# Performance work log

Measured on AMD Instinct MI355X. Metric: run time of the kernel, lower is better.

## Reference

```python
import jax, jax.numpy as jnp
import numpy as np

B, H, HF = 2048, 128, 10  # batch, bi-LSTM hidden, fc-LSTM hidden


def _lstm(x_seq, h0, c0, Wih, Whh, bih, bhh):
    """Unidirectional LSTM, PyTorch gate order (i, f, g, o).
    x_seq: [T, B, I]. Returns final (h, c), each [B, H].
    Input projection is hoisted out of the scan (one big GEMM)."""
    pre = jnp.einsum('tbi,gi->tbg', x_seq, Wih) + bih + bhh  # [T, B, 4H]

    def step(carry, p):
        h, c = carry
        g = p + h @ Whh.T
        i, f, gg, o = jnp.split(g, 4, axis=-1)
        c = jax.nn.sigmoid(f) * c + jax.nn.sigmoid(i) * jnp.tanh(gg)
        h = jax.nn.sigmoid(o) * jnp.tanh(c)
        return (h, c), None

    (hT, cT), _ = jax.lax.scan(step, (h0, c0), pre)
    return hT, cT


def setup_inputs() -> dict:
    key = jax.random.key(0)
    ks = iter(jax.random.split(key, 40))
    s = 1.0 / np.sqrt(H)
    sf = 1.0 / np.sqrt(HF)
    u = lambda shape, sc: jax.random.uniform(next(ks), shape, jnp.float32, -sc, sc)
    inp = {"x": jax.random.normal(next(ks), (B, 28, 28), jnp.float32)}
    for name in ["lr_f", "lr_b", "ud_f", "ud_b"]:
        inp["Wih_" + name] = u((4 * H, 28), s)
        inp["Whh_" + name] = u((4 * H, H), s)
        inp["bih_" + name] = u((4 * H,), s)
        inp["bhh_" + name] = u((4 * H,), s)
    inp["Wih_fc"] = u((4 * HF, 1), sf)
    inp["Whh_fc"] = u((4 * HF, HF), sf)
    inp["bih_fc"] = u((4 * HF,), sf)
    inp["bhh_fc"] = u((4 * HF,), sf)
    for name in ["h0_lr", "c0_lr", "h0_ud", "c0_ud"]:
        inp[name] = jax.random.normal(next(ks), (2, B, H), jnp.float32)
    inp["h0_fc"] = jax.random.normal(next(ks), (B, HF), jnp.float32)
    inp["c0_fc"] = jax.random.normal(next(ks), (B, HF), jnp.float32)
    return inp


def reference(x, Wih_lr_f, Whh_lr_f, bih_lr_f, bhh_lr_f,
              Wih_lr_b, Whh_lr_b, bih_lr_b, bhh_lr_b,
              Wih_ud_f, Whh_ud_f, bih_ud_f, bhh_ud_f,
              Wih_ud_b, Whh_ud_b, bih_ud_b, bhh_ud_b,
              Wih_fc, Whh_fc, bih_fc, bhh_fc,
              h0_lr, c0_lr, h0_ud, c0_ud, h0_fc, c0_fc):
    x_lr = jnp.transpose(x, (1, 0, 2))  # [28, B, 28]: rows as time
    x_ud = jnp.transpose(x, (2, 0, 1))  # [28, B, 28]: cols as time
    # bidirectional = forward scan + scan over reversed sequence
    h_lr_f, _ = _lstm(x_lr, h0_lr[0], c0_lr[0], Wih_lr_f, Whh_lr_f, bih_lr_f, bhh_lr_f)
    h_lr_b, _ = _lstm(x_lr[::-1], h0_lr[1], c0_lr[1], Wih_lr_b, Whh_lr_b, bih_lr_b, bhh_lr_b)
    h_ud_f, _ = _lstm(x_ud, h0_ud[0], c0_ud[0], Wih_ud_f, Whh_ud_f, bih_ud_f, bhh_ud_f)
    h_ud_b, _ = _lstm(x_ud[::-1], h0_ud[1], c0_ud[1], Wih_ud_b, Whh_ud_b, bih_ud_b, bhh_ud_b)
    feat = jnp.concatenate([h_lr_f, h_lr_b, h_ud_f, h_ud_b], axis=1)  # [B, 4H]
    seq = feat.T[:, :, None]  # [4H, B, 1]: feature index is the fc-LSTM time axis
    h_f, _ = _lstm(seq, h0_fc, c0_fc, Wih_fc, Whh_fc, bih_fc, bhh_fc)  # [B, 10]
    return jax.nn.log_softmax(h_f, axis=1)
```

## Files before the change

### kernel.cpp

```cpp
#include <hip/hip_runtime.h>
#include <hip/hip_bf16.h>

typedef __bf16 bf16x8 __attribute__((ext_vector_type(8)));
typedef float  f32x4  __attribute__((ext_vector_type(4)));

#define LOG2E 1.4426950408889634f
#define LN2   0.6931471805599453f

__device__ __forceinline__ float rcp_(float x){
#if __has_builtin(__builtin_amdgcn_rcpf)
  return __builtin_amdgcn_rcpf(x);
#else
  return 1.0f / x;
#endif
}
__device__ __forceinline__ float ex2_(float x){
#if __has_builtin(__builtin_amdgcn_exp2f)
  return __builtin_amdgcn_exp2f(x);
#else
  return exp2f(x);
#endif
}
__device__ __forceinline__ float lg2_(float x){
#if __has_builtin(__builtin_amdgcn_logf)
  return __builtin_amdgcn_logf(x);
#else
  return log2f(x);
#endif
}
__device__ __forceinline__ float sigp_(float xp){ return rcp_(1.0f + ex2_(xp)); }
__device__ __forceinline__ float tanp_(float gp){ return 1.0f - 2.0f*rcp_(1.0f + ex2_(gp)); }

struct LstmArgs {
  const float* Wih[4]; const float* Whh[4];
  const float* bih[4]; const float* bhh[4];
  const float* h0[4];  const float* c0[4];
};

__global__ void pack_weights(LstmArgs args, bf16x8* __restrict__ wpack,
                             float* __restrict__ bpack)
{
  const int idx = blockIdx.x*256 + threadIdx.x;
  if (idx >= 4*8*4*5*64) return;
  const int lane = idx & 63;
  int r = idx >> 6;
  const int kk = r % 5; r /= 5;
  const int g  = r & 3; r >>= 2;
  const int w  = r & 7;
  const int d  = r >> 3;
  const int lc = lane & 15, lr4 = lane >> 4;
  const int grow = g*128 + w*16 + lc;
  const float sc = (g == 2) ? 2.0f*LOG2E : -LOG2E;

  bf16x8 v;
  if (kk < 4){
    const float* p = args.Whh[d] + grow*128 + kk*32 + lr4*8;
#pragma unroll
    for (int j = 0; j < 8; ++j) v[j] = (__bf16)(p[j] * sc);
  } else {
#pragma unroll
    for (int j = 0; j < 8; ++j){
      const int xi = lr4*8 + j;
      v[j] = (xi < 28) ? (__bf16)(args.Wih[d][grow*28 + xi] * sc) : (__bf16)0.0f;
    }
  }
  wpack[idx] = v;
  if (kk == 0 && lr4 == 0)
    bpack[d*512 + grow] = (args.bih[d][grow] + args.bhh[d][grow]) * sc;
}

__global__ __launch_bounds__(512, 2) void lstm4_kernel(const float* __restrict__ x,
                                                       LstmArgs args,
                                                       const bf16x8* __restrict__ wpack,
                                                       const float* __restrict__ bpack,
                                                       __bf16* __restrict__ featB)
{
  const int dir = blockIdx.x >> 6;
  const int b0  = (blockIdx.x & 63) * 32;
  const int tid = threadIdx.x;
  const int w   = tid >> 6;
  const int l   = tid & 63;
  const int lc  = l & 15;
  const int lr4 = l >> 4;

  const float* __restrict__ h0 = args.h0[dir];
  const float* __restrict__ c0 = args.c0[dir];
  const int rev = dir & 1;
  const bool lrdir = (dir < 2);

  __shared__ __align__(16) __bf16 hcat[32 * 168];
  __shared__ __align__(16) __bf16 xstage[28 * 32 * 40];

  bf16x8 bfr[4][5];
  float  bias[4];
  {
    const bf16x8* wp = wpack + (dir*8 + w)*4*5*64;
#pragma unroll
    for (int g = 0; g < 4; ++g){
#pragma unroll
      for (int kk = 0; kk < 5; ++kk)
        bfr[g][kk] = wp[(g*5 + kk)*64 + l];
      bias[g] = bpack[dir*512 + g*128 + w*16 + lc];
    }
  }

  for (int idx = tid; idx < 32*196; idx += 512){
    const int row = idx / 196;
    const int rem = idx - row*196;
    if (lrdir){
      const int t = rem / 7, jg = rem - 7*t;
      const float4 v = *(const float4*)&x[(b0+row)*784 + t*28 + jg*4];
      __bf16* dst = &xstage[(t*32 + row)*40 + jg*4];
      dst[0]=(__bf16)v.x; dst[1]=(__bf16)v.y; dst[2]=(__bf16)v.z; dst[3]=(__bf16)v.w;
    } else {
      const int j = rem / 7, tg = rem - 7*j;
      const float4 v = *(const float4*)&x[(b0+row)*784 + j*28 + tg*4];
      xstage[((tg*4+0)*32 + row)*40 + j] = (__bf16)v.x;
      xstage[((tg*4+1)*32 + row)*40 + j] = (__bf16)v.y;
      xstage[((tg*4+2)*32 + row)*40 + j] = (__bf16)v.z;
      xstage[((tg*4+3)*32 + row)*40 + j] = (__bf16)v.w;
    }
  }
  for (int idx = tid; idx < 28*32; idx += 512){
    const int t = idx >> 5, row = idx & 31;
    __bf16* p = &xstage[(t*32 + row)*40 + 28];
    p[0] = p[1] = p[2] = p[3] = (__bf16)0.0f;
  }

  float cst[2][4], hfin[2][4];
#pragma unroll
  for (int m = 0; m < 2; ++m)
#pragma unroll
  for (int r = 0; r < 4; ++r){
    const int row = 16*m + 4*lr4 + r;
    const int col = w*16 + lc;
    cst[m][r] = c0[(b0+row)*128 + col];
    hcat[row*168 + col] = (__bf16)h0[(b0+row)*128 + col];
    hfin[m][r] = 0.0f;
  }

  for (int s = 0; s < 28; ++s){
    const int t = rev ? (27 - s) : s;
    __syncthreads();

    f32x4 acc[2][4];
#pragma unroll
    for (int m = 0; m < 2; ++m)
#pragma unroll
    for (int g = 0; g < 4; ++g){
      f32x4 bv = {bias[g], bias[g], bias[g], bias[g]};
      acc[m][g] = bv;
    }
#pragma unroll
    for (int m = 0; m < 2; ++m){
#pragma unroll
      for (int kk = 0; kk < 5; ++kk){
        const bf16x8 a = (kk < 4)
          ? *(const bf16x8*)&hcat[(16*m + lc)*168 + kk*32 + lr4*8]
          : *(const bf16x8*)&xstage[(t*32 + 16*m + lc)*40 + lr4*8];
#pragma unroll
        for (int g = 0; g < 4; ++g)
          acc[m][g] = __builtin_amdgcn_mfma_f32_16x16x32_bf16(a, bfr[g][kk], acc[m][g], 0, 0, 0);
      }
    }
    __syncthreads();

#pragma unroll
    for (int m = 0; m < 2; ++m)
#pragma unroll
    for (int r = 0; r < 4; ++r){
      const float cc = sigp_(acc[m][1][r])*cst[m][r] + sigp_(acc[m][0][r])*tanp_(acc[m][2][r]);
      cst[m][r] = cc;
      const float hv = sigp_(acc[m][3][r])*tanp_(2.0f*LOG2E*cc);
      hfin[m][r] = hv;
      hcat[(16*m + 4*lr4 + r)*168 + w*16 + lc] = (__bf16)hv;
    }
  }

  {
    const int fcol = dir*128 + w*16 + lc;
#pragma unroll
    for (int m = 0; m < 2; ++m)
#pragma unroll
    for (int r = 0; r < 4; ++r)
      featB[(b0 + 16*m + 4*lr4 + r)*512 + fcol] = (__bf16)hfin[m][r];
  }
}

__global__ __launch_bounds__(256) void fc_lstm_wave(const ushort* __restrict__ featB,
                                                    const float* __restrict__ Wih,
                                                    const float* __restrict__ Whh,
                                                    const float* __restrict__ bih,
                                                    const float* __restrict__ bhh,
                                                    const float* __restrict__ h0,
                                                    const float* __restrict__ c0,
                                                    float* __restrict__ out)
{
  const int tid = threadIdx.x;
  const int l   = tid & 63;
  const int e   = blockIdx.x*4 + (tid >> 6);
  const int u   = l >> 2;
  const int g   = l & 3;
  const int uc  = (u < 10) ? u : 9;
  const bool valid = (u < 10);
  const float sc = (g == 2) ? 2.0f*LOG2E : -LOG2E;
  const int row = g*10 + uc;

  float wh[10];
#pragma unroll
  for (int m = 0; m < 10; ++m) wh[m] = valid ? Whh[row*10 + m]*sc : 0.0f;
  const float wx   = valid ? Wih[row]*sc : 0.0f;
  const float bia  = valid ? (bih[row] + bhh[row])*sc : 0.0f;
  const float actA = (g == 2) ? 1.0f : 0.0f;
  const float actB = (g == 2) ? -2.0f : 1.0f;

  float c = valid ? c0[e*10 + uc] : 0.0f;
  float hlast = valid ? h0[e*10 + uc] : 0.0f;

  int hb = __float_as_int(hlast);
  float sh0 = __int_as_float(__builtin_amdgcn_readlane(hb,  0));
  float sh1 = __int_as_float(__builtin_amdgcn_readlane(hb,  4));
  float sh2 = __int_as_float(__builtin_amdgcn_readlane(hb,  8));
  float sh3 = __int_as_float(__builtin_amdgcn_readlane(hb, 12));
  float sh4 = __int_as_float(__builtin_amdgcn_readlane(hb, 16));
  float sh5 = __int_as_float(__builtin_amdgcn_readlane(hb, 20));
  float sh6 = __int_as_float(__builtin_amdgcn_readlane(hb, 24));
  float sh7 = __int_as_float(__builtin_amdgcn_readlane(hb, 28));
  float sh8 = __int_as_float(__builtin_amdgcn_readlane(hb, 32));
  float sh9 = __int_as_float(__builtin_amdgcn_readlane(hb, 36));

  const ushort* fB = featB + e*512;
  int vxc = (int)fB[l];
  int vxn = (int)fB[64 + l];

  for (int win = 0; win < 8; ++win){
#pragma unroll 4
    for (int j = 0; j < 64; ++j){
      const float xs = __int_as_float(__builtin_amdgcn_readlane(vxc, j) << 16);
      float a0 = __builtin_fmaf(wx, xs, bia);
      a0 = __builtin_fmaf(wh[0], sh0, a0);
      float a1 = wh[1]*sh1;
      a0 = __builtin_fmaf(wh[2], sh2, a0); a1 = __builtin_fmaf(wh[3], sh3, a1);
      a0 = __builtin_fmaf(wh[4], sh4, a0); a1 = __builtin_fmaf(wh[5], sh5, a1);
      a0 = __builtin_fmaf(wh[6], sh6, a0); a1 = __builtin_fmaf(wh[7], sh7, a1);
      a0 = __builtin_fmaf(wh[8], sh8, a0); a1 = __builtin_fmaf(wh[9], sh9, a1);
      const float acc = a0 + a1;
      const float rc  = rcp_(1.0f + ex2_(acc));
      const float val = __builtin_fmaf(actB, rc, actA);
      const int   vi  = __float_as_int(val);
      const float si  = __int_as_float(__builtin_amdgcn_mov_dpp(vi, 0x00, 0xF, 0xF, false));
      const float sf  = __int_as_float(__builtin_amdgcn_mov_dpp(vi, 0x55, 0xF, 0xF, false));
      const float tg  = __int_as_float(__builtin_amdgcn_mov_dpp(vi, 0xAA, 0xF, 0xF, false));
      const float so  = __int_as_float(__builtin_amdgcn_mov_dpp(vi, 0xFF, 0xF, 0xF, false));
      c = __builtin_fmaf(sf, c, si*tg);
      const float tc = __builtin_fmaf(-2.0f, rcp_(1.0f + ex2_(2.0f*LOG2E*c)), 1.0f);
      const float h  = so*tc;
      hlast = h;
      const int hbi = __float_as_int(h);
      sh0 = __int_as_float(__builtin_amdgcn_readlane(hbi,  0));
      sh1 = __int_as_float(__builtin_amdgcn_readlane(hbi,  4));
      sh2 = __int_as_float(__builtin_amdgcn_readlane(hbi,  8));
      sh3 = __int_as_float(__builtin_amdgcn_readlane(hbi, 12));
      sh4 = __int_as_float(__builtin_amdgcn_readlane(hbi, 16));
      sh5 = __int_as_float(__builtin_amdgcn_readlane(hbi, 20));
      sh6 = __int_as_float(__builtin_amdgcn_readlane(hbi, 24));
      sh7 = __int_as_float(__builtin_amdgcn_readlane(hbi, 28));
      sh8 = __int_as_float(__builtin_amdgcn_readlane(hbi, 32));
      sh9 = __int_as_float(__builtin_amdgcn_readlane(hbi, 36));
    }
    vxc = vxn;
    if (win < 6) vxn = (int)fB[(win+2)*64 + l];
  }

  float mx = sh0;
  mx = fmaxf(mx, sh1); mx = fmaxf(mx, sh2); mx = fmaxf(mx, sh3);
  mx = fmaxf(mx, sh4); mx = fmaxf(mx, sh5); mx = fmaxf(mx, sh6);
  mx = fmaxf(mx, sh7); mx = fmaxf(mx, sh8); mx = fmaxf(mx, sh9);
  float es = ex2_(LOG2E*(sh0 - mx));
  es += ex2_(LOG2E*(sh1 - mx)); es += ex2_(LOG2E*(sh2 - mx));
  es += ex2_(LOG2E*(sh3 - mx)); es += ex2_(LOG2E*(sh4 - mx));
  es += ex2_(LOG2E*(sh5 - mx)); es += ex2_(LOG2E*(sh6 - mx));
  es += ex2_(LOG2E*(sh7 - mx)); es += ex2_(LOG2E*(sh8 - mx));
  es += ex2_(LOG2E*(sh9 - mx));
  const float lse = LN2 * lg2_(es);
  if (valid && g == 0) out[e*10 + u] = hlast - mx - lse;
}

extern "C" void kernel_launch(void* const* d_in, const int* in_sizes, int n_in,
                              void* d_out, int out_size, void* d_ws, size_t ws_size,
                              hipStream_t stream)
{
  const float* x = (const float*)d_in[0];
  LstmArgs a;
  const int base[4] = {1, 5, 9, 13};
  for (int d = 0; d < 4; ++d){
    a.Wih[d] = (const float*)d_in[base[d] + 0];
    a.Whh[d] = (const float*)d_in[base[d] + 1];
    a.bih[d] = (const float*)d_in[base[d] + 2];
    a.bhh[d] = (const float*)d_in[base[d] + 3];
  }
  const float* h0lr = (const float*)d_in[21];
  const float* c0lr = (const float*)d_in[22];
  const float* h0ud = (const float*)d_in[23];
  const float* c0ud = (const float*)d_in[24];
  a.h0[0] = h0lr;               a.c0[0] = c0lr;
  a.h0[1] = h0lr + 2048*128;    a.c0[1] = c0lr + 2048*128;
  a.h0[2] = h0ud;               a.c0[2] = c0ud;
  a.h0[3] = h0ud + 2048*128;    a.c0[3] = c0ud + 2048*128;

  char* ws = (char*)d_ws;
  __bf16* featB = (__bf16*)ws;
  bf16x8* wpack = (bf16x8*)(ws + (2u<<20));
  float*  bpack = (float*)(ws + (2u<<20) + 655360u);

  pack_weights<<<160, 256, 0, stream>>>(a, wpack, bpack);
  lstm4_kernel<<<256, 512, 0, stream>>>(x, a, wpack, bpack, featB);
  fc_lstm_wave<<<512, 256, 0, stream>>>((const ushort*)featB,
      (const float*)d_in[17], (const float*)d_in[18],
      (const float*)d_in[19], (const float*)d_in[20],
      (const float*)d_in[25], (const float*)d_in[26],
      (float*)d_out);
}
```

Measured before the change: 142.1 us.

## Halve LSTM batch tile with double-buffered h, interleave two fc-LSTM sequences per wave

The bi-LSTM kernel now handles 16 batch rows per block instead of 32, launching twice as many blocks at higher occupancy. The hidden-state buffer is double-buffered so each timestep needs one barrier instead of two. The fc-LSTM kernel now runs two independent sequences per wave, interleaved to hide the latency of the serial recurrence, and launches half as many blocks. The cost is more per-wave register pressure in the fc kernel and per-block fixed overhead (weight fragment loads) paid twice as often in the bi-LSTM kernel.

Measured after the change: 160.4 us. 12.9% more time.

```diff
diff --git a/kernel.cpp b/kernel.cpp
--- a/kernel.cpp
+++ b/kernel.cpp
@@ -69,14 +69,14 @@
     bpack[d*512 + grow] = (args.bih[d][grow] + args.bhh[d][grow]) * sc;
 }
 
-__global__ __launch_bounds__(512, 2) void lstm4_kernel(const float* __restrict__ x,
+__global__ __launch_bounds__(512, 4) void lstm4_kernel(const float* __restrict__ x,
                                                        LstmArgs args,
                                                        const bf16x8* __restrict__ wpack,
                                                        const float* __restrict__ bpack,
                                                        __bf16* __restrict__ featB)
 {
-  const int dir = blockIdx.x >> 6;
-  const int b0  = (blockIdx.x & 63) * 32;
+  const int dir = blockIdx.x >> 7;
+  const int b0  = (blockIdx.x & 127) * 16;
   const int tid = threadIdx.x;
   const int w   = tid >> 6;
   const int l   = tid & 63;
@@ -88,8 +88,8 @@
   const int rev = dir & 1;
   const bool lrdir = (dir < 2);
 
-  __shared__ __align__(16) __bf16 hcat[32 * 168];
-  __shared__ __align__(16) __bf16 xstage[28 * 32 * 40];
+  __shared__ __align__(16) __bf16 hcat[2][16 * 168];
+  __shared__ __align__(16) __bf16 xstage[28 * 16 * 40];
 
   bf16x8 bfr[4][5];
   float  bias[4];
@@ -104,86 +104,77 @@
     }
   }
 
-  for (int idx = tid; idx < 32*196; idx += 512){
+  for (int idx = tid; idx < 16*196; idx += 512){
     const int row = idx / 196;
     const int rem = idx - row*196;
     if (lrdir){
       const int t = rem / 7, jg = rem - 7*t;
       const float4 v = *(const float4*)&x[(b0+row)*784 + t*28 + jg*4];
-      __bf16* dst = &xstage[(t*32 + row)*40 + jg*4];
+      __bf16* dst = &xstage[(t*16 + row)*40 + jg*4];
       dst[0]=(__bf16)v.x; dst[1]=(__bf16)v.y; dst[2]=(__bf16)v.z; dst[3]=(__bf16)v.w;
     } else {
       const int j = rem / 7, tg = rem - 7*j;
       const float4 v = *(const float4*)&x[(b0+row)*784 + j*28 + tg*4];
-      xstage[((tg*4+0)*32 + row)*40 + j] = (__bf16)v.x;
-      xstage[((tg*4+1)*32 + row)*40 + j] = (__bf16)v.y;
-      xstage[((tg*4+2)*32 + row)*40 + j] = (__bf16)v.z;
-      xstage[((tg*4+3)*32 + row)*40 + j] = (__bf16)v.w;
-    }
-  }
-  for (int idx = tid; idx < 28*32; idx += 512){
-    const int t = idx >> 5, row = idx & 31;
-    __bf16* p = &xstage[(t*32 + row)*40 + 28];
+      xstage[((tg*4+0)*16 + row)*40 + j] = (__bf16)v.x;
+      xstage[((tg*4+1)*16 + row)*40 + j] = (__bf16)v.y;
+      xstage[((tg*4+2)*16 + row)*40 + j] = (__bf16)v.z;
+      xstage[((tg*4+3)*16 + row)*40 + j] = (__bf16)v.w;
+    }
+  }
+  if (tid < 28*16){
+    const int t = tid >> 4, row = tid & 15;
+    __bf16* p = &xstage[(t*16 + row)*40 + 28];
     p[0] = p[1] = p[2] = p[3] = (__bf16)0.0f;
   }
 
-  float cst[2][4], hfin[2][4];
-#pragma unroll
-  for (int m = 0; m < 2; ++m)
+  float cst[4], hfin[4];
 #pragma unroll
   for (int r = 0; r < 4; ++r){
-    const int row = 16*m + 4*lr4 + r;
+    const int row = 4*lr4 + r;
     const int col = w*16 + lc;
-    cst[m][r] = c0[(b0+row)*128 + col];
-    hcat[row*168 + col] = (__bf16)h0[(b0+row)*128 + col];
-    hfin[m][r] = 0.0f;
-  }
-
+    cst[r] = c0[(b0+row)*128 + col];
+    hcat[0][row*168 + col] = (__bf16)h0[(b0+row)*128 + col];
+    hfin[r] = 0.0f;
+  }
+  __syncthreads();
+
+  int cur = 0;
   for (int s = 0; s < 28; ++s){
     const int t = rev ? (27 - s) : s;
-    __syncthreads();
-
-    f32x4 acc[2][4];
-#pragma unroll
-    for (int m = 0; m < 2; ++m)
+
+    f32x4 acc[4];
 #pragma unroll
     for (int g = 0; g < 4; ++g){
       f32x4 bv = {bias[g], bias[g], bias[g], bias[g]};
-      acc[m][g] = bv;
-    }
-#pragma unroll
-    for (int m = 0; m < 2; ++m){
-#pragma unroll
-      for (int kk = 0; kk < 5; ++kk){
-        const bf16x8 a = (kk < 4)
-          ? *(const bf16x8*)&hcat[(16*m + lc)*168 + kk*32 + lr4*8]
-          : *(const bf16x8*)&xstage[(t*32 + 16*m + lc)*40 + lr4*8];
-#pragma unroll
-        for (int g = 0; g < 4; ++g)
-          acc[m][g] = __builtin_amdgcn_mfma_f32_16x16x32_bf16(a, bfr[g][kk], acc[m][g], 0, 0, 0);
-      }
+      acc[g] = bv;
+    }
+#pragma unroll
+    for (int kk = 0; kk < 5; ++kk){
+      const bf16x8 a = (kk < 4)
+        ? *(const bf16x8*)&hcat[cur][lc*168 + kk*32 + lr4*8]
+        : *(const bf16x8*)&xstage[(t*16 + lc)*40 + lr4*8];
+#pragma unroll
+      for (int g = 0; g < 4; ++g)
+        acc[g] = __builtin_amdgcn_mfma_f32_16x16x32_bf16(a, bfr[g][kk], acc[g], 0, 0, 0);
+    }
+
+#pragma unroll
+    for (int r = 0; r < 4; ++r){
+      const float cc = sigp_(acc[1][r])*cst[r] + sigp_(acc[0][r])*tanp_(acc[2][r]);
+      cst[r] = cc;
+      const float hv = sigp_(acc[3][r])*tanp_(2.0f*LOG2E*cc);
+      hfin[r] = hv;
+      hcat[cur^1][(4*lr4 + r)*168 + w*16 + lc] = (__bf16)hv;
     }
     __syncthreads();
-
-#pragma unroll
-    for (int m = 0; m < 2; ++m)
-#pragma unroll
-    for (int r = 0; r < 4; ++r){
-      const float cc = sigp_(acc[m][1][r])*cst[m][r] + sigp_(acc[m][0][r])*tanp_(acc[m][2][r]);
-      cst[m][r] = cc;
-      const float hv = sigp_(acc[m][3][r])*tanp_(2.0f*LOG2E*cc);
-      hfin[m][r] = hv;
-      hcat[(16*m + 4*lr4 + r)*168 + w*16 + lc] = (__bf16)hv;
-    }
+    cur ^= 1;
   }
 
   {
     const int fcol = dir*128 + w*16 + lc;
 #pragma unroll
-    for (int m = 0; m < 2; ++m)
-#pragma unroll
     for (int r = 0; r < 4; ++r)
-      featB[(b0 + 16*m + 4*lr4 + r)*512 + fcol] = (__bf16)hfin[m][r];
+      featB[(b0 + 4*lr4 + r)*512 + fcol] = (__bf16)hfin[r];
   }
 }
 
@@ -198,7 +189,7 @@
 {
   const int tid = threadIdx.x;
   const int l   = tid & 63;
-  const int e   = blockIdx.x*4 + (tid >> 6);
+  const int e0  = (blockIdx.x*4 + (tid >> 6)) * 2;
   const int u   = l >> 2;
   const int g   = l & 3;
   const int uc  = (u < 10) ? u : 9;
@@ -214,76 +205,71 @@
   const float actA = (g == 2) ? 1.0f : 0.0f;
   const float actB = (g == 2) ? -2.0f : 1.0f;
 
-  float c = valid ? c0[e*10 + uc] : 0.0f;
-  float hlast = valid ? h0[e*10 + uc] : 0.0f;
-
-  int hb = __float_as_int(hlast);
-  float sh0 = __int_as_float(__builtin_amdgcn_readlane(hb,  0));
-  float sh1 = __int_as_float(__builtin_amdgcn_readlane(hb,  4));
-  float sh2 = __int_as_float(__builtin_amdgcn_readlane(hb,  8));
-  float sh3 = __int_as_float(__builtin_amdgcn_readlane(hb, 12));
-  float sh4 = __int_as_float(__builtin_amdgcn_readlane(hb, 16));
-  float sh5 = __int_as_float(__builtin_amdgcn_readlane(hb, 20));
-  float sh6 = __int_as_float(__builtin_amdgcn_readlane(hb, 24));
-  float sh7 = __int_as_float(__builtin_amdgcn_readlane(hb, 28));
-  float sh8 = __int_as_float(__builtin_amdgcn_readlane(hb, 32));
-  float sh9 = __int_as_float(__builtin_amdgcn_readlane(hb, 36));
-
-  const ushort* fB = featB + e*512;
-  int vxc = (int)fB[l];
-  int vxn = (int)fB[64 + l];
+  float c[2], hlast[2];
+  float sh[2][10];
+  int   vxc[2], vxn[2];
+#pragma unroll
+  for (int E = 0; E < 2; ++E){
+    const int e = e0 + E;
+    c[E]     = valid ? c0[e*10 + uc] : 0.0f;
+    hlast[E] = valid ? h0[e*10 + uc] : 0.0f;
+    const int hb = __float_as_int(hlast[E]);
+#pragma unroll
+    for (int m = 0; m < 10; ++m)
+      sh[E][m] = __int_as_float(__builtin_amdgcn_readlane(hb, 4*m));
+    vxc[E] = (int)featB[e*512 + l];
+    vxn[E] = (int)featB[e*512 + 64 + l];
+  }
 
   for (int win = 0; win < 8; ++win){
-#pragma unroll 4
+#pragma unroll 2
     for (int j = 0; j < 64; ++j){
-      const float xs = __int_as_float(__builtin_amdgcn_readlane(vxc, j) << 16);
-      float a0 = __builtin_fmaf(wx, xs, bia);
-      a0 = __builtin_fmaf(wh[0], sh0, a0);
-      float a1 = wh[1]*sh1;
-      a0 = __builtin_fmaf(wh[2], sh2, a0); a1 = __builtin_fmaf(wh[3], sh3, a1);
-      a0 = __builtin_fmaf(wh[4], sh4, a0); a1 = __builtin_fmaf(wh[5], sh5, a1);
-      a0 = __builtin_fmaf(wh[6], sh6, a0); a1 = __builtin_fmaf(wh[7], sh7, a1);
-      a0 = __builtin_fmaf(wh[8], sh8, a0); a1 = __builtin_fmaf(wh[9], sh9, a1);
-      const float acc = a0 + a1;
-      const float rc  = rcp_(1.0f + ex2_(acc));
-      const float val = __builtin_fmaf(actB, rc, actA);
-      const int   vi  = __float_as_int(val);
-      const float si  = __int_as_float(__builtin_amdgcn_mov_dpp(vi, 0x00, 0xF, 0xF, false));
-      const float sf  = __int_as_float(__builtin_amdgcn_mov_dpp(vi, 0x55, 0xF, 0xF, false));
-      const float tg  = __int_as_float(__builtin_amdgcn_mov_dpp(vi, 0xAA, 0xF, 0xF, false));
-      const float so  = __int_as_float(__builtin_amdgcn_mov_dpp(vi, 0xFF, 0xF, 0xF, false));
-      c = __builtin_fmaf(sf, c, si*tg);
-      const float tc = __builtin_fmaf(-2.0f, rcp_(1.0f + ex2_(2.0f*LOG2E*c)), 1.0f);
-      const float h  = so*tc;
-      hlast = h;
-      const int hbi = __float_as_int(h);
-      sh0 = __int_as_float(__builtin_amdgcn_readlane(hbi,  0));
-      sh1 = __int_as_float(__builtin_amdgcn_readlane(hbi,  4));
-      sh2 = __int_as_float(__builtin_amdgcn_readlane(hbi,  8));
-      sh3 = __int_as_float(__builtin_amdgcn_readlane(hbi, 12));
-      sh4 = __int_as_float(__builtin_amdgcn_readlane(hbi, 16));
-      sh5 = __int_as_float(__builtin_amdgcn_readlane(hbi, 20));
-      sh6 = __int_as_float(__builtin_amdgcn_readlane(hbi, 24));
-      sh7 = __int_as_float(__builtin_amdgcn_readlane(hbi, 28));
-      sh8 = __int_as_float(__builtin_amdgcn_readlane(hbi, 32));
-      sh9 = __int_as_float(__builtin_amdgcn_readlane(hbi, 36));
-    }
-    vxc = vxn;
-    if (win < 6) vxn = (int)fB[(win+2)*64 + l];
-  }
-
-  float mx = sh0;
-  mx = fmaxf(mx, sh1); mx = fmaxf(mx, sh2); mx = fmaxf(mx, sh3);
-  mx = fmaxf(mx, sh4); mx = fmaxf(mx, sh5); mx = fmaxf(mx, sh6);
-  mx = fmaxf(mx, sh7); mx = fmaxf(mx, sh8); mx = fmaxf(mx, sh9);
-  float es = ex2_(LOG2E*(sh0 - mx));
-  es += ex2_(LOG2E*(sh1 - mx)); es += ex2_(LOG2E*(sh2 - mx));
-  es += ex2_(LOG2E*(sh3 - mx)); es += ex2_(LOG2E*(sh4 - mx));
-  es += ex2_(LOG2E*(sh5 - mx)); es += ex2_(LOG2E*(sh6 - mx));
-  es += ex2_(LOG2E*(sh7 - mx)); es += ex2_(LOG2E*(sh8 - mx));
-  es += ex2_(LOG2E*(sh9 - mx));
-  const float lse = LN2 * lg2_(es);
-  if (valid && g == 0) out[e*10 + u] = hlast - mx - lse;
+#pragma unroll
+      for (int E = 0; E < 2; ++E){
+        const float xs = __int_as_float(__builtin_amdgcn_readlane(vxc[E], j) << 16);
+        float a0 = __builtin_fmaf(wx, xs, bia);
+        a0 = __builtin_fmaf(wh[0], sh[E][0], a0);
+        float a1 = wh[1]*sh[E][1];
+        a0 = __builtin_fmaf(wh[2], sh[E][2], a0); a1 = __builtin_fmaf(wh[3], sh[E][3], a1);
+        a0 = __builtin_fmaf(wh[4], sh[E][4], a0); a1 = __builtin_fmaf(wh[5], sh[E][5], a1);
+        a0 = __builtin_fmaf(wh[6], sh[E][6], a0); a1 = __builtin_fmaf(wh[7], sh[E][7], a1);
+        a0 = __builtin_fmaf(wh[8], sh[E][8], a0); a1 = __builtin_fmaf(wh[9], sh[E][9], a1);
+        const float acc = a0 + a1;
+        const float rc  = rcp_(1.0f + ex2_(acc));
+        const float val = __builtin_fmaf(actB, rc, actA);
+        const int   vi  = __float_as_int(val);
+        const float si  = __int_as_float(__builtin_amdgcn_mov_dpp(vi, 0x00, 0xF, 0xF, false));
+        const float sf  = __int_as_float(__builtin_amdgcn_mov_dpp(vi, 0x55, 0xF, 0xF, false));
+        const float tg  = __int_as_float(__builtin_amdgcn_mov_dpp(vi, 0xAA, 0xF, 0xF, false));
+        const float so  = __int_as_float(__builtin_amdgcn_mov_dpp(vi, 0xFF, 0xF, 0xF, false));
+        c[E] = __builtin_fmaf(sf, c[E], si*tg);
+        const float tc = __builtin_fmaf(-2.0f, rcp_(1.0f + ex2_(2.0f*LOG2E*c[E])), 1.0f);
+        const float h  = so*tc;
+        hlast[E] = h;
+        const int hbi = __float_as_int(h);
+#pragma unroll
+        for (int m = 0; m < 10; ++m)
+          sh[E][m] = __int_as_float(__builtin_amdgcn_readlane(hbi, 4*m));
+      }
+    }
+#pragma unroll
+    for (int E = 0; E < 2; ++E){
+      vxc[E] = vxn[E];
+      if (win < 6) vxn[E] = (int)featB[(e0+E)*512 + (win+2)*64 + l];
+    }
+  }
+
+#pragma unroll
+  for (int E = 0; E < 2; ++E){
+    float mx = sh[E][0];
+#pragma unroll
+    for (int m = 1; m < 10; ++m) mx = fmaxf(mx, sh[E][m]);
+    float es = 0.0f;
+#pragma unroll
+    for (int m = 0; m < 10; ++m) es += ex2_(LOG2E*(sh[E][m] - mx));
+    const float lse = LN2 * lg2_(es);
+    if (valid && g == 0) out[(e0+E)*10 + u] = hlast[E] - mx - lse;
+  }
 }
 
 extern "C" void kernel_launch(void* const* d_in, const int* in_sizes, int n_in,
@@ -314,8 +300,8 @@
   float*  bpack = (float*)(ws + (2u<<20) + 655360u);
 
   pack_weights<<<160, 256, 0, stream>>>(a, wpack, bpack);
-  lstm4_kernel<<<256, 512, 0, stream>>>(x, a, wpack, bpack, featB);
-  fc_lstm_wave<<<512, 256, 0, stream>>>((const ushort*)featB,
+  lstm4_kernel<<<512, 512, 0, stream>>>(x, a, wpack, bpack, featB);
+  fc_lstm_wave<<<256, 256, 0, stream>>>((const ushort*)featB,
       (const float*)d_in[17], (const float*)d_in[18],
       (const float*)d_in[19], (const float*)d_in[20],
       (const float*)d_in[25], (const float*)d_in[26],
```

## Double-buffer hidden state, merge gate reciprocals, use packed fp16 dot in fc LSTM

Applied to the files above, without the earlier changes.

In the bi-LSTM kernel the hidden-state tile in shared memory is now double-buffered, which drops one of the two barriers per timestep. The gate math is reworked to share reciprocals across sigmoid/tanh pairs, and the final features are written with vectorized 16-byte stores taken from shared memory. In the fc LSTM the recurrent weights and hidden values are packed into fp16 pairs and combined with fdot2, halving the readlanes and FMAs on the serial critical path. The cost is reduced precision from fp16 round-toward-zero packing and a possible overflow risk when the exponentials are multiplied together.

Measured after the change: 139.7 us. About the same (-1.7%).

```diff
diff --git a/kernel.cpp b/kernel.cpp
--- a/kernel.cpp
+++ b/kernel.cpp
@@ -1,8 +1,9 @@
 #include <hip/hip_runtime.h>
 #include <hip/hip_bf16.h>
 
-typedef __bf16 bf16x8 __attribute__((ext_vector_type(8)));
-typedef float  f32x4  __attribute__((ext_vector_type(4)));
+typedef __bf16   bf16x8 __attribute__((ext_vector_type(8)));
+typedef float    f32x4  __attribute__((ext_vector_type(4)));
+typedef _Float16 h16x2  __attribute__((ext_vector_type(2)));
 
 #define LOG2E 1.4426950408889634f
 #define LN2   0.6931471805599453f
@@ -30,6 +31,25 @@
 }
 __device__ __forceinline__ float sigp_(float xp){ return rcp_(1.0f + ex2_(xp)); }
 __device__ __forceinline__ float tanp_(float gp){ return 1.0f - 2.0f*rcp_(1.0f + ex2_(gp)); }
+
+__device__ __forceinline__ int pkrtz_(float a, float b){
+  auto v = __builtin_amdgcn_cvt_pkrtz(a, b);
+  int r; __builtin_memcpy(&r, &v, 4); return r;
+}
+__device__ __forceinline__ h16x2 as_h2_(int x){
+  h16x2 r; __builtin_memcpy(&r, &x, 4); return r;
+}
+
+#if __has_builtin(__builtin_amdgcn_fdot2)
+__device__ __forceinline__ float fdot2_(int w, int h, float a){
+  return __builtin_amdgcn_fdot2(as_h2_(w), as_h2_(h), a, false);
+}
+#else
+__device__ __forceinline__ float fdot2_(int w, int h, float a){
+  h16x2 wv = as_h2_(w), hv = as_h2_(h);
+  return a + (float)wv[0]*(float)hv[0] + (float)wv[1]*(float)hv[1];
+}
+#endif
 
 struct LstmArgs {
   const float* Wih[4]; const float* Whh[4];
@@ -88,7 +108,7 @@
   const int rev = dir & 1;
   const bool lrdir = (dir < 2);
 
-  __shared__ __align__(16) __bf16 hcat[32 * 168];
+  __shared__ __align__(16) __bf16 hcat[2][32 * 168];
   __shared__ __align__(16) __bf16 xstage[28 * 32 * 40];
 
   bf16x8 bfr[4][5];
@@ -127,7 +147,7 @@
     p[0] = p[1] = p[2] = p[3] = (__bf16)0.0f;
   }
 
-  float cst[2][4], hfin[2][4];
+  float cst[2][4];
 #pragma unroll
   for (int m = 0; m < 2; ++m)
 #pragma unroll
@@ -135,13 +155,14 @@
     const int row = 16*m + 4*lr4 + r;
     const int col = w*16 + lc;
     cst[m][r] = c0[(b0+row)*128 + col];
-    hcat[row*168 + col] = (__bf16)h0[(b0+row)*128 + col];
-    hfin[m][r] = 0.0f;
-  }
-
+    hcat[0][row*168 + col] = (__bf16)h0[(b0+row)*128 + col];
+  }
+  __syncthreads();
+
+  int cur = 0;
   for (int s = 0; s < 28; ++s){
     const int t = rev ? (27 - s) : s;
-    __syncthreads();
+    const int nxt = cur ^ 1;
 
     f32x4 acc[2][4];
 #pragma unroll
@@ -156,34 +177,40 @@
 #pragma unroll
       for (int kk = 0; kk < 5; ++kk){
         const bf16x8 a = (kk < 4)
-          ? *(const bf16x8*)&hcat[(16*m + lc)*168 + kk*32 + lr4*8]
+          ? *(const bf16x8*)&hcat[cur][(16*m + lc)*168 + kk*32 + lr4*8]
           : *(const bf16x8*)&xstage[(t*32 + 16*m + lc)*40 + lr4*8];
 #pragma unroll
         for (int g = 0; g < 4; ++g)
           acc[m][g] = __builtin_amdgcn_mfma_f32_16x16x32_bf16(a, bfr[g][kk], acc[m][g], 0, 0, 0);
       }
     }
+
+#pragma unroll
+    for (int m = 0; m < 2; ++m)
+#pragma unroll
+    for (int r = 0; r < 4; ++r){
+      const float Ei = ex2_(acc[m][0][r]);
+      const float Ef = ex2_(acc[m][1][r]);
+      const float Eg = ex2_(acc[m][2][r]);
+      const float Eo = ex2_(acc[m][3][r]);
+      const float rf  = rcp_(1.0f + Ef);
+      const float rig = rcp_((1.0f + Ei)*(1.0f + Eg));
+      const float cc  = rf*cst[m][r] + (Eg - 1.0f)*rig;
+      cst[m][r] = cc;
+      const float Ec  = ex2_(2.0f*LOG2E*cc);
+      const float roc = rcp_((1.0f + Eo)*(1.0f + Ec));
+      const float hv  = (Ec - 1.0f)*roc;
+      hcat[nxt][(16*m + 4*lr4 + r)*168 + w*16 + lc] = (__bf16)hv;
+    }
     __syncthreads();
-
-#pragma unroll
-    for (int m = 0; m < 2; ++m)
-#pragma unroll
-    for (int r = 0; r < 4; ++r){
-      const float cc = sigp_(acc[m][1][r])*cst[m][r] + sigp_(acc[m][0][r])*tanp_(acc[m][2][r]);
-      cst[m][r] = cc;
-      const float hv = sigp_(acc[m][3][r])*tanp_(2.0f*LOG2E*cc);
-      hfin[m][r] = hv;
-      hcat[(16*m + 4*lr4 + r)*168 + w*16 + lc] = (__bf16)hv;
-    }
+    cur = nxt;
   }
 
   {
-    const int fcol = dir*128 + w*16 + lc;
-#pragma unroll
-    for (int m = 0; m < 2; ++m)
-#pragma unroll
-    for (int r = 0; r < 4; ++r)
-      featB[(b0 + 16*m + 4*lr4 + r)*512 + fcol] = (__bf16)hfin[m][r];
+    const int row = tid >> 4;
+    const int cg  = tid & 15;
+    const bf16x8 hv = *(const bf16x8*)&hcat[cur][row*168 + cg*8];
+    *(bf16x8*)&featB[(b0+row)*512 + dir*128 + cg*8] = hv;
   }
 }
 
@@ -206,28 +233,32 @@
   const float sc = (g == 2) ? 2.0f*LOG2E : -LOG2E;
   const int row = g*10 + uc;
 
-  float wh[10];
-#pragma unroll
-  for (int m = 0; m < 10; ++m) wh[m] = valid ? Whh[row*10 + m]*sc : 0.0f;
+  int wh2[5];
+#pragma unroll
+  for (int m = 0; m < 5; ++m){
+    const float w0 = valid ? Whh[row*10 + 2*m]   * sc : 0.0f;
+    const float w1 = valid ? Whh[row*10 + 2*m+1] * sc : 0.0f;
+    wh2[m] = pkrtz_(w0, w1);
+  }
   const float wx   = valid ? Wih[row]*sc : 0.0f;
   const float bia  = valid ? (bih[row] + bhh[row])*sc : 0.0f;
   const float actA = (g == 2) ? 1.0f : 0.0f;
   const float actB = (g == 2) ? -2.0f : 1.0f;
 
-  float c = valid ? c0[e*10 + uc] : 0.0f;
+  float c     = valid ? c0[e*10 + uc] : 0.0f;
   float hlast = valid ? h0[e*10 + uc] : 0.0f;
 
-  int hb = __float_as_int(hlast);
-  float sh0 = __int_as_float(__builtin_amdgcn_readlane(hb,  0));
-  float sh1 = __int_as_float(__builtin_amdgcn_readlane(hb,  4));
-  float sh2 = __int_as_float(__builtin_amdgcn_readlane(hb,  8));
-  float sh3 = __int_as_float(__builtin_amdgcn_readlane(hb, 12));
-  float sh4 = __int_as_float(__builtin_amdgcn_readlane(hb, 16));
-  float sh5 = __int_as_float(__builtin_amdgcn_readlane(hb, 20));
-  float sh6 = __int_as_float(__builtin_amdgcn_readlane(hb, 24));
-  float sh7 = __int_as_float(__builtin_amdgcn_readlane(hb, 28));
-  float sh8 = __int_as_float(__builtin_amdgcn_readlane(hb, 32));
-  float sh9 = __int_as_float(__builtin_amdgcn_readlane(hb, 36));
+  int hp0, hp1, hp2, hp3, hp4;
+  {
+    const float hnb = __int_as_float(
+        __builtin_amdgcn_ds_swizzle(__float_as_int(hlast), 0x101F));
+    const int hpi = pkrtz_(hlast, hnb);
+    hp0 = __builtin_amdgcn_readlane(hpi,  0);
+    hp1 = __builtin_amdgcn_readlane(hpi,  8);
+    hp2 = __builtin_amdgcn_readlane(hpi, 16);
+    hp3 = __builtin_amdgcn_readlane(hpi, 24);
+    hp4 = __builtin_amdgcn_readlane(hpi, 32);
+  }
 
   const ushort* fB = featB + e*512;
   int vxc = (int)fB[l];
@@ -238,12 +269,11 @@
     for (int j = 0; j < 64; ++j){
       const float xs = __int_as_float(__builtin_amdgcn_readlane(vxc, j) << 16);
       float a0 = __builtin_fmaf(wx, xs, bia);
-      a0 = __builtin_fmaf(wh[0], sh0, a0);
-      float a1 = wh[1]*sh1;
-      a0 = __builtin_fmaf(wh[2], sh2, a0); a1 = __builtin_fmaf(wh[3], sh3, a1);
-      a0 = __builtin_fmaf(wh[4], sh4, a0); a1 = __builtin_fmaf(wh[5], sh5, a1);
-      a0 = __builtin_fmaf(wh[6], sh6, a0); a1 = __builtin_fmaf(wh[7], sh7, a1);
-      a0 = __builtin_fmaf(wh[8], sh8, a0); a1 = __builtin_fmaf(wh[9], sh9, a1);
+      a0 = fdot2_(wh2[0], hp0, a0);
+      float a1 = fdot2_(wh2[1], hp1, 0.0f);
+      a0 = fdot2_(wh2[2], hp2, a0);
+      a1 = fdot2_(wh2[3], hp3, a1);
+      a0 = fdot2_(wh2[4], hp4, a0);
       const float acc = a0 + a1;
       const float rc  = rcp_(1.0f + ex2_(acc));
       const float val = __builtin_fmaf(actB, rc, actA);
@@ -256,32 +286,30 @@
       const float tc = __builtin_fmaf(-2.0f, rcp_(1.0f + ex2_(2.0f*LOG2E*c)), 1.0f);
       const float h  = so*tc;
       hlast = h;
-      const int hbi = __float_as_int(h);
-      sh0 = __int_as_float(__builtin_amdgcn_readlane(hbi,  0));
-      sh1 = __int_as_float(__builtin_amdgcn_readlane(hbi,  4));
-      sh2 = __int_as_float(__builtin_amdgcn_readlane(hbi,  8));
-      sh3 = __int_as_float(__builtin_amdgcn_readlane(hbi, 12));
-      sh4 = __int_as_float(__builtin_amdgcn_readlane(hbi, 16));
-      sh5 = __int_as_float(__builtin_amdgcn_readlane(hbi, 20));
-      sh6 = __int_as_float(__builtin_amdgcn_readlane(hbi, 24));
-      sh7 = __int_as_float(__builtin_amdgcn_readlane(hbi, 28));
-      sh8 = __int_as_float(__builtin_amdgcn_readlane(hbi, 32));
-      sh9 = __int_as_float(__builtin_amdgcn_readlane(hbi, 36));
+      const float hnb = __int_as_float(
+          __builtin_amdgcn_ds_swizzle(__float_as_int(h), 0x101F));
+      const int hpi = pkrtz_(h, hnb);
+      hp0 = __builtin_amdgcn_readlane(hpi,  0);
+      hp1 = __builtin_amdgcn_readlane(hpi,  8);
+      hp2 = __builtin_amdgcn_readlane(hpi, 16);
+      hp3 = __builtin_amdgcn_readlane(hpi, 24);
+      hp4 = __builtin_amdgcn_readlane(hpi, 32);
     }
     vxc = vxn;
     if (win < 6) vxn = (int)fB[(win+2)*64 + l];
   }
 
-  float mx = sh0;
-  mx = fmaxf(mx, sh1); mx = fmaxf(mx, sh2); mx = fmaxf(mx, sh3);
-  mx = fmaxf(mx, sh4); mx = fmaxf(mx, sh5); mx = fmaxf(mx, sh6);
-  mx = fmaxf(mx, sh7); mx = fmaxf(mx, sh8); mx = fmaxf(mx, sh9);
-  float es = ex2_(LOG2E*(sh0 - mx));
-  es += ex2_(LOG2E*(sh1 - mx)); es += ex2_(LOG2E*(sh2 - mx));
-  es += ex2_(LOG2E*(sh3 - mx)); es += ex2_(LOG2E*(sh4 - mx));
-  es += ex2_(LOG2E*(sh5 - mx)); es += ex2_(LOG2E*(sh6 - mx));
-  es += ex2_(LOG2E*(sh7 - mx)); es += ex2_(LOG2E*(sh8 - mx));
-  es += ex2_(LOG2E*(sh9 - mx));
+  const int hb = __float_as_int(hlast);
+  float sh[10];
+#pragma unroll
+  for (int m = 0; m < 10; ++m)
+    sh[m] = __int_as_float(__builtin_amdgcn_readlane(hb, 4*m));
+  float mx = sh[0];
+#pragma unroll
+  for (int m = 1; m < 10; ++m) mx = fmaxf(mx, sh[m]);
+  float es = 0.0f;
+#pragma unroll
+  for (int m = 0; m < 10; ++m) es += ex2_(LOG2E*(sh[m] - mx));
   const float lse = LN2 * lg2_(es);
   if (valid && g == 0) out[e*10 + u] = hlast - mx - lse;
 }
```

## Double-buffer LSTM hidden state, merge gate reciprocals, shorten fc dependency chain

Applied to the files above, without the earlier changes.

The bi-LSTM kernel now ping-pongs the hidden-state tile between two shared buffers, which removes one of the two per-step barriers. The gate math merges reciprocals by computing sigmoid(i)*tanh(g) and sigmoid(o)*tanh(c) with a single rcp on a product of denominators, cutting transcendental ops per element. Final features are written from shared memory with vectorized 16-byte stores instead of scattered scalar stores. In the fc LSTM, the 10-term dot product is split into four shorter FMA chains and the unroll factor is raised to 8; the merged reciprocals risk overflow when the exponentials become large.

New measurement: 137.7 us. -3.0%, faster.

```diff
diff --git a/kernel.cpp b/kernel.cpp
--- a/kernel.cpp
+++ b/kernel.cpp
@@ -1,8 +1,8 @@
 #include <hip/hip_runtime.h>
 #include <hip/hip_bf16.h>
 
-typedef __bf16 bf16x8 __attribute__((ext_vector_type(8)));
-typedef float  f32x4  __attribute__((ext_vector_type(4)));
+typedef __bf16   bf16x8 __attribute__((ext_vector_type(8)));
+typedef float    f32x4  __attribute__((ext_vector_type(4)));
 
 #define LOG2E 1.4426950408889634f
 #define LN2   0.6931471805599453f
@@ -28,8 +28,6 @@
   return log2f(x);
 #endif
 }
-__device__ __forceinline__ float sigp_(float xp){ return rcp_(1.0f + ex2_(xp)); }
-__device__ __forceinline__ float tanp_(float gp){ return 1.0f - 2.0f*rcp_(1.0f + ex2_(gp)); }
 
 struct LstmArgs {
   const float* Wih[4]; const float* Whh[4];
@@ -88,7 +86,7 @@
   const int rev = dir & 1;
   const bool lrdir = (dir < 2);
 
-  __shared__ __align__(16) __bf16 hcat[32 * 168];
+  __shared__ __align__(16) __bf16 hcat[2][32 * 168];
   __shared__ __align__(16) __bf16 xstage[28 * 32 * 40];
 
   bf16x8 bfr[4][5];
@@ -127,7 +125,7 @@
     p[0] = p[1] = p[2] = p[3] = (__bf16)0.0f;
   }
 
-  float cst[2][4], hfin[2][4];
+  float cst[2][4];
 #pragma unroll
   for (int m = 0; m < 2; ++m)
 #pragma unroll
@@ -135,13 +133,14 @@
     const int row = 16*m + 4*lr4 + r;
     const int col = w*16 + lc;
     cst[m][r] = c0[(b0+row)*128 + col];
-    hcat[row*168 + col] = (__bf16)h0[(b0+row)*128 + col];
-    hfin[m][r] = 0.0f;
-  }
-
+    hcat[0][row*168 + col] = (__bf16)h0[(b0+row)*128 + col];
+  }
+  __syncthreads();
+
+  int cur = 0;
   for (int s = 0; s < 28; ++s){
     const int t = rev ? (27 - s) : s;
-    __syncthreads();
+    const int nxt = cur ^ 1;
 
     f32x4 acc[2][4];
 #pragma unroll
@@ -156,34 +155,40 @@
 #pragma unroll
       for (int kk = 0; kk < 5; ++kk){
         const bf16x8 a = (kk < 4)
-          ? *(const bf16x8*)&hcat[(16*m + lc)*168 + kk*32 + lr4*8]
+          ? *(const bf16x8*)&hcat[cur][(16*m + lc)*168 + kk*32 + lr4*8]
           : *(const bf16x8*)&xstage[(t*32 + 16*m + lc)*40 + lr4*8];
 #pragma unroll
         for (int g = 0; g < 4; ++g)
           acc[m][g] = __builtin_amdgcn_mfma_f32_16x16x32_bf16(a, bfr[g][kk], acc[m][g], 0, 0, 0);
       }
     }
+
+#pragma unroll
+    for (int m = 0; m < 2; ++m)
+#pragma unroll
+    for (int r = 0; r < 4; ++r){
+      const float Ei = ex2_(acc[m][0][r]);
+      const float Ef = ex2_(acc[m][1][r]);
+      const float Eg = ex2_(acc[m][2][r]);
+      const float Eo = ex2_(acc[m][3][r]);
+      const float rf  = rcp_(1.0f + Ef);
+      const float rig = rcp_((1.0f + Ei)*(1.0f + Eg));
+      const float cc  = rf*cst[m][r] + (Eg - 1.0f)*rig;
+      cst[m][r] = cc;
+      const float Ec  = ex2_(2.0f*LOG2E*cc);
+      const float roc = rcp_((1.0f + Eo)*(1.0f + Ec));
+      const float hv  = (Ec - 1.0f)*roc;
+      hcat[nxt][(16*m + 4*lr4 + r)*168 + w*16 + lc] = (__bf16)hv;
+    }
     __syncthreads();
-
-#pragma unroll
-    for (int m = 0; m < 2; ++m)
-#pragma unroll
-    for (int r = 0; r < 4; ++r){
-      const float cc = sigp_(acc[m][1][r])*cst[m][r] + sigp_(acc[m][0][r])*tanp_(acc[m][2][r]);
-      cst[m][r] = cc;
-      const float hv = sigp_(acc[m][3][r])*tanp_(2.0f*LOG2E*cc);
-      hfin[m][r] = hv;
-      hcat[(16*m + 4*lr4 + r)*168 + w*16 + lc] = (__bf16)hv;
-    }
+    cur = nxt;
   }
 
   {
-    const int fcol = dir*128 + w*16 + lc;
-#pragma unroll
-    for (int m = 0; m < 2; ++m)
-#pragma unroll
-    for (int r = 0; r < 4; ++r)
-      featB[(b0 + 16*m + 4*lr4 + r)*512 + fcol] = (__bf16)hfin[m][r];
+    const int row = tid >> 4;
+    const int cg  = tid & 15;
+    const bf16x8 hv = *(const bf16x8*)&hcat[cur][row*168 + cg*8];
+    *(bf16x8*)&featB[(b0+row)*512 + dir*128 + cg*8] = hv;
   }
 }
 
@@ -214,37 +219,44 @@
   const float actA = (g == 2) ? 1.0f : 0.0f;
   const float actB = (g == 2) ? -2.0f : 1.0f;
 
-  float c = valid ? c0[e*10 + uc] : 0.0f;
+  float c     = valid ? c0[e*10 + uc] : 0.0f;
   float hlast = valid ? h0[e*10 + uc] : 0.0f;
 
-  int hb = __float_as_int(hlast);
-  float sh0 = __int_as_float(__builtin_amdgcn_readlane(hb,  0));
-  float sh1 = __int_as_float(__builtin_amdgcn_readlane(hb,  4));
-  float sh2 = __int_as_float(__builtin_amdgcn_readlane(hb,  8));
-  float sh3 = __int_as_float(__builtin_amdgcn_readlane(hb, 12));
-  float sh4 = __int_as_float(__builtin_amdgcn_readlane(hb, 16));
-  float sh5 = __int_as_float(__builtin_amdgcn_readlane(hb, 20));
-  float sh6 = __int_as_float(__builtin_amdgcn_readlane(hb, 24));
-  float sh7 = __int_as_float(__builtin_amdgcn_readlane(hb, 28));
-  float sh8 = __int_as_float(__builtin_amdgcn_readlane(hb, 32));
-  float sh9 = __int_as_float(__builtin_amdgcn_readlane(hb, 36));
+  float sh0, sh1, sh2, sh3, sh4, sh5, sh6, sh7, sh8, sh9;
+  {
+    const int hb = __float_as_int(hlast);
+    sh0 = __int_as_float(__builtin_amdgcn_readlane(hb,  0));
+    sh1 = __int_as_float(__builtin_amdgcn_readlane(hb,  4));
+    sh2 = __int_as_float(__builtin_amdgcn_readlane(hb,  8));
+    sh3 = __int_as_float(__builtin_amdgcn_readlane(hb, 12));
+    sh4 = __int_as_float(__builtin_amdgcn_readlane(hb, 16));
+    sh5 = __int_as_float(__builtin_amdgcn_readlane(hb, 20));
+    sh6 = __int_as_float(__builtin_amdgcn_readlane(hb, 24));
+    sh7 = __int_as_float(__builtin_amdgcn_readlane(hb, 28));
+    sh8 = __int_as_float(__builtin_amdgcn_readlane(hb, 32));
+    sh9 = __int_as_float(__builtin_amdgcn_readlane(hb, 36));
+  }
 
   const ushort* fB = featB + e*512;
   int vxc = (int)fB[l];
   int vxn = (int)fB[64 + l];
 
   for (int win = 0; win < 8; ++win){
-#pragma unroll 4
+#pragma unroll 8
     for (int j = 0; j < 64; ++j){
       const float xs = __int_as_float(__builtin_amdgcn_readlane(vxc, j) << 16);
       float a0 = __builtin_fmaf(wx, xs, bia);
       a0 = __builtin_fmaf(wh[0], sh0, a0);
-      float a1 = wh[1]*sh1;
-      a0 = __builtin_fmaf(wh[2], sh2, a0); a1 = __builtin_fmaf(wh[3], sh3, a1);
-      a0 = __builtin_fmaf(wh[4], sh4, a0); a1 = __builtin_fmaf(wh[5], sh5, a1);
-      a0 = __builtin_fmaf(wh[6], sh6, a0); a1 = __builtin_fmaf(wh[7], sh7, a1);
-      a0 = __builtin_fmaf(wh[8], sh8, a0); a1 = __builtin_fmaf(wh[9], sh9, a1);
-      const float acc = a0 + a1;
+      a0 = __builtin_fmaf(wh[1], sh1, a0);
+      float a1 = wh[2]*sh2;
+      a1 = __builtin_fmaf(wh[3], sh3, a1);
+      a1 = __builtin_fmaf(wh[4], sh4, a1);
+      float a2 = wh[5]*sh5;
+      a2 = __builtin_fmaf(wh[6], sh6, a2);
+      a2 = __builtin_fmaf(wh[7], sh7, a2);
+      float a3 = wh[8]*sh8;
+      a3 = __builtin_fmaf(wh[9], sh9, a3);
+      const float acc = (a0 + a1) + (a2 + a3);
       const float rc  = rcp_(1.0f + ex2_(acc));
       const float val = __builtin_fmaf(actB, rc, actA);
       const int   vi  = __float_as_int(val);
```
